# Optimization experiments

Measured on AMD Instinct MI355X. Metric: run time of the kernel, lower is better.

The kernel has to match this reference:

```python
import jax, jax.numpy as jnp
import numpy as np

B, T, I, H, F1, C = 65536, 30, 26, 24, 8, 4  # batch, seq_len, input, hidden, fc1, classes


def setup_inputs() -> dict:
    key = jax.random.key(0)
    ks = jax.random.split(key, 9)
    s_ih = 1.0 / np.sqrt(H)
    return {
        "x": jax.random.normal(ks[0], (B, T, I), dtype=jnp.float32),
        "W_ih": jax.random.uniform(ks[1], (3 * H, I), jnp.float32, -s_ih, s_ih),
        "W_hh": jax.random.uniform(ks[2], (3 * H, H), jnp.float32, -s_ih, s_ih),
        "b_ih": jax.random.uniform(ks[3], (3 * H,), jnp.float32, -s_ih, s_ih),
        "b_hh": jax.random.uniform(ks[4], (3 * H,), jnp.float32, -s_ih, s_ih),
        "fc1_w": jax.random.normal(ks[5], (F1, H), jnp.float32) * 0.1,
        "fc1_b": jax.random.normal(ks[6], (F1,), jnp.float32) * 0.1,
        "fc2_w": jax.random.normal(ks[7], (C, F1), jnp.float32) * 0.1,
        "fc2_b": jax.random.normal(ks[8], (C,), jnp.float32) * 0.1,
    }


def reference(x, W_ih, W_hh, b_ih, b_hh, fc1_w, fc1_b, fc2_w, fc2_b):
    # Precompute input projections for all timesteps: (B, T, 3H)
    xp = jnp.einsum("bti,gi->btg", x, W_ih) + b_ih

    def step(h, xt):  # h: (B,H), xt: (B,3H)
        gh = h @ W_hh.T + b_hh  # (B, 3H)
        xr, xz, xn = jnp.split(xt, 3, axis=-1)
        hr, hz, hn = jnp.split(gh, 3, axis=-1)
        r = jax.nn.sigmoid(xr + hr)
        z = jax.nn.sigmoid(xz + hz)
        n = jnp.tanh(xn + r * hn)
        h_new = (1.0 - z) * n + z * h
        return h_new, None

    h0 = jnp.zeros((x.shape[0], W_hh.shape[1]), dtype=x.dtype)
    h, _ = jax.lax.scan(step, h0, jnp.swapaxes(xp, 0, 1))  # final hidden (B, H)

    # eval mode: dropout is identity
    hid = jax.nn.relu(h @ fc1_w.T + fc1_b)
    logits = hid @ fc2_w.T + fc2_b
    return jax.nn.softmax(logits, axis=1)
```

## Files before the change

kernel.cpp:

```cpp
#include <hip/hip_runtime.h>

typedef __bf16 bf16x8 __attribute__((ext_vector_type(8)));
typedef float f32x4 __attribute__((ext_vector_type(4)));
typedef float f32x2 __attribute__((ext_vector_type(2)));

#define T_SEQ 30
#define NIN 26
#define XPITCH 780

#define W_IH 0
#define W_HH 1872
#define B_IH 3600
#define B_HH 3672
#define FC1W 3744
#define FC1B 3936
#define FC2W 3944
#define FC2B 3976

__device__ __forceinline__ float fast_sigmoid(float x) {
    return __builtin_amdgcn_rcpf(1.f + __expf(-x));
}
__device__ __forceinline__ float fast_tanh(float x) {
    return 2.f * __builtin_amdgcn_rcpf(1.f + __expf(-2.f * x)) - 1.f;
}

__global__ __launch_bounds__(256, 4) void gru_kernel(
    const float* __restrict__ x, const float* __restrict__ W_ih,
    const float* __restrict__ W_hh, const float* __restrict__ b_ih,
    const float* __restrict__ b_hh, const float* __restrict__ fc1_w,
    const float* __restrict__ fc1_b, const float* __restrict__ fc2_w,
    const float* __restrict__ fc2_b, float* __restrict__ out)
{
    __shared__ float wbuf[3980];
    __shared__ __attribute__((aligned(16))) __bf16 hbuf[4 * 512];

    const int tid = threadIdx.x;
    const int lane = tid & 63;
    const int wid = tid >> 6;
    const int m = lane & 15;
    const int kg = lane >> 4;
    const int w16 = wid << 4;
    const int b0 = blockIdx.x << 6;

    for (int i = tid; i < 1872; i += 256) wbuf[W_IH + i] = W_ih[i];
    for (int i = tid; i < 1728; i += 256) wbuf[W_HH + i] = W_hh[i];
    if (tid < 72) wbuf[B_IH + tid] = b_ih[tid];
    else if (tid < 144) wbuf[B_IH + tid] = b_hh[tid - 72];
    if (tid < 192) wbuf[FC1W + tid] = fc1_w[tid];
    if (tid < 8)   wbuf[FC1B + tid] = fc1_b[tid];
    if (tid < 32)  wbuf[FC2W + tid] = fc2_w[tid];
    if (tid < 4)   wbuf[FC2B + tid] = fc2_b[tid];
    for (int i = tid; i < 2048; i += 256) hbuf[i] = (__bf16)0.f;
    __syncthreads();

    bf16x8 bIh[6], bHh[6];
    float bxc[6], bhc[6];
    #pragma unroll
    for (int Tn = 0; Tn < 6; ++Tn) {
        const int np = Tn * 16 + m;
        const int gp = np >> 5;
        const int jh = np & 31;
        const bool vc = jh < 24;
        const int g = gp * 24 + jh;
        #pragma unroll
        for (int e = 0; e < 8; ++e) {
            const int k = kg * 8 + e;
            const float vi = (vc && k < 26) ? wbuf[W_IH + g * 26 + k] : 0.f;
            const float vh = (vc && k < 24) ? wbuf[W_HH + g * 24 + k] : 0.f;
            bIh[Tn][e] = (__bf16)vi;
            bHh[Tn][e] = (__bf16)vh;
        }
        bxc[Tn] = vc ? wbuf[B_IH + g] : 0.f;
        bhc[Tn] = vc ? wbuf[B_HH + g] : 0.f;
    }
    const float brz0 = bxc[0] + bhc[0], brz1 = bxc[1] + bhc[1];
    const float brz2 = bxc[2] + bhc[2], brz3 = bxc[3] + bhc[3];

    __bf16* hw = &hbuf[wid * 512];

    const float* px = x + (size_t)(b0 + w16 + m) * XPITCH + ((kg < 3) ? kg * 8 : 24);
    const bool full = (kg < 3);

    f32x2 zero2 = {0.f, 0.f};
    f32x2 xc0, xc1, xc2, xc3;
    xc1 = zero2; xc2 = zero2; xc3 = zero2;
    xc0 = *(const f32x2*)px;
    if (full) {
        xc1 = *(const f32x2*)(px + 2);
        xc2 = *(const f32x2*)(px + 4);
        xc3 = *(const f32x2*)(px + 6);
    }

    f32x4 hc0 = {0.f, 0.f, 0.f, 0.f}, hc1 = {0.f, 0.f, 0.f, 0.f};
    const f32x4 z4 = {0.f, 0.f, 0.f, 0.f};

    const int ra  = m * 32 + ((kg ^ (m >> 2)) << 3);
    const int wr0 = (kg * 4) * 32 + ((((m >> 3) ^ kg) & 3) << 3) + (m & 7);
    const int wr1 = (kg * 4) * 32 + (((2 ^ kg) & 3) << 3) + m;

    #pragma unroll 2
    for (int t = 0; t < T_SEQ; ++t) {
        f32x2 xn0, xn1, xn2, xn3;
        xn0 = zero2; xn1 = zero2; xn2 = zero2; xn3 = zero2;
        if (t < T_SEQ - 1) {
            const float* p = px + (t + 1) * NIN;
            xn0 = *(const f32x2*)p;
            if (full) {
                xn1 = *(const f32x2*)(p + 2);
                xn2 = *(const f32x2*)(p + 4);
                xn3 = *(const f32x2*)(p + 6);
            }
        }

        bf16x8 ax;
        ax[0] = (__bf16)xc0.x; ax[1] = (__bf16)xc0.y;
        ax[2] = (__bf16)xc1.x; ax[3] = (__bf16)xc1.y;
        ax[4] = (__bf16)xc2.x; ax[5] = (__bf16)xc2.y;
        ax[6] = (__bf16)xc3.x; ax[7] = (__bf16)xc3.y;

        const bf16x8 ah = *(const bf16x8*)&hw[ra];

        {
            f32x4 xr = __builtin_amdgcn_mfma_f32_16x16x32_bf16(ax, bIh[0], z4, 0, 0, 0);
            f32x4 hr = __builtin_amdgcn_mfma_f32_16x16x32_bf16(ah, bHh[0], z4, 0, 0, 0);
            f32x4 xz = __builtin_amdgcn_mfma_f32_16x16x32_bf16(ax, bIh[2], z4, 0, 0, 0);
            f32x4 hz = __builtin_amdgcn_mfma_f32_16x16x32_bf16(ah, bHh[2], z4, 0, 0, 0);
            f32x4 xn_ = __builtin_amdgcn_mfma_f32_16x16x32_bf16(ax, bIh[4], z4, 0, 0, 0);
            f32x4 hn = __builtin_amdgcn_mfma_f32_16x16x32_bf16(ah, bHh[4], z4, 0, 0, 0);
            #pragma unroll
            for (int r = 0; r < 4; ++r) {
                const float rg = fast_sigmoid(xr[r] + hr[r] + brz0);
                const float zg = fast_sigmoid(xz[r] + hz[r] + brz2);
                const float ng = fast_tanh(xn_[r] + bxc[4] + rg * (hn[r] + bhc[4]));
                hc0[r] = ng + zg * (hc0[r] - ng);
            }
            #pragma unroll
            for (int r = 0; r < 4; ++r)
                hw[wr0 + r * 32] = (__bf16)hc0[r];
        }

        {
            f32x4 xr = __builtin_amdgcn_mfma_f32_16x16x32_bf16(ax, bIh[1], z4, 0, 0, 0);
            f32x4 hr = __builtin_amdgcn_mfma_f32_16x16x32_bf16(ah, bHh[1], z4, 0, 0, 0);
            f32x4 xz = __builtin_amdgcn_mfma_f32_16x16x32_bf16(ax, bIh[3], z4, 0, 0, 0);
            f32x4 hz = __builtin_amdgcn_mfma_f32_16x16x32_bf16(ah, bHh[3], z4, 0, 0, 0);
            f32x4 xn_ = __builtin_amdgcn_mfma_f32_16x16x32_bf16(ax, bIh[5], z4, 0, 0, 0);
            f32x4 hn = __builtin_amdgcn_mfma_f32_16x16x32_bf16(ah, bHh[5], z4, 0, 0, 0);
            #pragma unroll
            for (int r = 0; r < 4; ++r) {
                const float rg = fast_sigmoid(xr[r] + hr[r] + brz1);
                const float zg = fast_sigmoid(xz[r] + hz[r] + brz3);
                const float ng = fast_tanh(xn_[r] + bxc[5] + rg * (hn[r] + bhc[5]));
                hc1[r] = ng + zg * (hc1[r] - ng);
            }
            if (m < 8) {
                #pragma unroll
                for (int r = 0; r < 4; ++r)
                    hw[wr1 + r * 32] = (__bf16)hc1[r];
            }
        }

        xc0 = xn0; xc1 = xn1; xc2 = xn2; xc3 = xn3;
    }

    if (lane < 16) {
        const int row = lane;
        float hv[24];
        #pragma unroll
        for (int j = 0; j < 24; ++j)
            hv[j] = (float)hw[row * 32 + ((((j >> 3) ^ (row >> 2)) & 3) << 3) + (j & 7)];
        float lg[4] = {wbuf[FC2B], wbuf[FC2B + 1], wbuf[FC2B + 2], wbuf[FC2B + 3]};
        #pragma unroll
        for (int o = 0; o < 8; ++o) {
            float s = wbuf[FC1B + o];
            #pragma unroll
            for (int j = 0; j < 24; ++j) s += wbuf[FC1W + o * 24 + j] * hv[j];
            s = fmaxf(s, 0.f);
            #pragma unroll
            for (int c = 0; c < 4; ++c) lg[c] += wbuf[FC2W + c * 8 + o] * s;
        }
        const float mx = fmaxf(fmaxf(lg[0], lg[1]), fmaxf(lg[2], lg[3]));
        const float e0 = __expf(lg[0] - mx), e1 = __expf(lg[1] - mx);
        const float e2 = __expf(lg[2] - mx), e3 = __expf(lg[3] - mx);
        const float inv = __builtin_amdgcn_rcpf(e0 + e1 + e2 + e3);
        f32x4 pr = {e0 * inv, e1 * inv, e2 * inv, e3 * inv};
        *(f32x4*)&out[(size_t)(b0 + w16 + row) * 4] = pr;
    }
}

extern "C" void kernel_launch(void* const* d_in, const int* in_sizes, int n_in,
                              void* d_out, int out_size, void* d_ws, size_t ws_size,
                              hipStream_t stream) {
    const float* xx    = (const float*)d_in[0];
    const float* w_ih  = (const float*)d_in[1];
    const float* w_hh  = (const float*)d_in[2];
    const float* bih   = (const float*)d_in[3];
    const float* bhh   = (const float*)d_in[4];
    const float* f1w   = (const float*)d_in[5];
    const float* f1b   = (const float*)d_in[6];
    const float* f2w   = (const float*)d_in[7];
    const float* f2b   = (const float*)d_in[8];
    float* outp = (float*)d_out;

    dim3 grid(65536 / 64), block(256);
    gru_kernel<<<grid, block, 0, stream>>>(xx, w_ih, w_hh, bih, bhh, f1w, f1b, f2w, f2b, outp);
}
```

Measured before the change: 323.0 us.

## Stage whole x tile into LDS as bf16 with coalesced loads, fold log2e

Instead of each lane fetching its x slice from global memory every timestep with strided 8-byte loads, the block cooperatively loads the entire 32-row x tile with contiguous row loads, converts it to bf16 and stores it in swizzled shared memory. The second half of the sequence is staged during the first timesteps to overlap loading with the recurrence. The block shrinks to 128 threads covering 32 rows, and weights are read directly from global memory instead of through LDS. Gate weights and biases are prescaled by log2e so sigmoid and tanh use a raw exp2 instruction. The cost is about 50KB of LDS per block, which limits occupancy, plus an extra barrier inside the time loop.

```diff
diff --git a/kernel.cpp b/kernel.cpp
--- a/kernel.cpp
+++ b/kernel.cpp
@@ -7,32 +7,46 @@
 #define T_SEQ 30
 #define NIN 26
 #define XPITCH 780
-
-#define W_IH 0
-#define W_HH 1872
-#define B_IH 3600
-#define B_HH 3672
-#define FC1W 3744
-#define FC1B 3936
-#define FC2W 3944
-#define FC2B 3976
-
-__device__ __forceinline__ float fast_sigmoid(float x) {
-    return __builtin_amdgcn_rcpf(1.f + __expf(-x));
+#define LOG2E 1.44269504088896340736f
+
+__device__ __forceinline__ float sig2(float s) {
+    return __builtin_amdgcn_rcpf(1.f + __builtin_amdgcn_exp2f(-s));
 }
-__device__ __forceinline__ float fast_tanh(float x) {
-    return 2.f * __builtin_amdgcn_rcpf(1.f + __expf(-2.f * x)) - 1.f;
-}
-
-__global__ __launch_bounds__(256, 4) void gru_kernel(
+
+#define LOADC(BUF, c, half) do {                                              \
+    const int rr_ = (c) / 15, tt_ = (c) % 15 + (half) * 15;                   \
+    const float* sp_ = x + (size_t)(b0 + rr_) * XPITCH + tt_ * NIN;           \
+    _Pragma("unroll") for (int q_ = 0; q_ < 13; ++q_)                         \
+        BUF[q_] = *(const f32x2*)(sp_ + 2 * q_);                              \
+} while (0)
+
+#define WRITEC(BUF, c, half) do {                                             \
+    const int rr_ = (c) / 15, tt_ = (c) % 15 + (half) * 15;                   \
+    const int id_ = rr_ * 30 + tt_;                                           \
+    const int ix_ = (id_ ^ ((rr_ >> 2) & 3)) << 3;                            \
+    _Pragma("unroll") for (int kk_ = 0; kk_ < 3; ++kk_) {                     \
+        bf16x8 wv_;                                                           \
+        _Pragma("unroll") for (int q_ = 0; q_ < 4; ++q_) {                    \
+            wv_[2 * q_]     = (__bf16)BUF[kk_ * 4 + q_].x;                    \
+            wv_[2 * q_ + 1] = (__bf16)BUF[kk_ * 4 + q_].y;                    \
+        }                                                                     \
+        *(bf16x8*)&xmain[kk_ * 7680 + ix_] = wv_;                             \
+    }                                                                         \
+    xtail[id_ * 2]     = (__bf16)BUF[12].x;                                   \
+    xtail[id_ * 2 + 1] = (__bf16)BUF[12].y;                                   \
+} while (0)
+
+__global__ __launch_bounds__(128, 2) void gru_kernel(
     const float* __restrict__ x, const float* __restrict__ W_ih,
     const float* __restrict__ W_hh, const float* __restrict__ b_ih,
     const float* __restrict__ b_hh, const float* __restrict__ fc1_w,
     const float* __restrict__ fc1_b, const float* __restrict__ fc2_w,
     const float* __restrict__ fc2_b, float* __restrict__ out)
 {
-    __shared__ float wbuf[3980];
-    __shared__ __attribute__((aligned(16))) __bf16 hbuf[4 * 512];
+    __shared__ __attribute__((aligned(16))) __bf16 xmain[23040];
+    __shared__ __attribute__((aligned(8)))  __bf16 xtail[1920];
+    __shared__ __attribute__((aligned(16))) __bf16 hbuf[1024];
+    __shared__ float wbuf[236];
 
     const int tid = threadIdx.x;
     const int lane = tid & 63;
@@ -40,23 +54,23 @@
     const int m = lane & 15;
     const int kg = lane >> 4;
     const int w16 = wid << 4;
-    const int b0 = blockIdx.x << 6;
-
-    for (int i = tid; i < 1872; i += 256) wbuf[W_IH + i] = W_ih[i];
-    for (int i = tid; i < 1728; i += 256) wbuf[W_HH + i] = W_hh[i];
-    if (tid < 72) wbuf[B_IH + tid] = b_ih[tid];
-    else if (tid < 144) wbuf[B_IH + tid] = b_hh[tid - 72];
-    if (tid < 192) wbuf[FC1W + tid] = fc1_w[tid];
-    if (tid < 8)   wbuf[FC1B + tid] = fc1_b[tid];
-    if (tid < 32)  wbuf[FC2W + tid] = fc2_w[tid];
-    if (tid < 4)   wbuf[FC2B + tid] = fc2_b[tid];
-    for (int i = tid; i < 2048; i += 256) hbuf[i] = (__bf16)0.f;
-    __syncthreads();
+    const int b0 = blockIdx.x << 5;
+
+    for (int i = tid; i < 236; i += 128) {
+        float v;
+        if (i < 192) v = fc1_w[i];
+        else if (i < 200) v = fc1_b[i - 192];
+        else if (i < 232) v = fc2_w[i - 200];
+        else v = fc2_b[i - 232];
+        wbuf[i] = v;
+    }
+    for (int i = tid; i < 1024; i += 128) hbuf[i] = (__bf16)0.f;
 
     bf16x8 bIh[6], bHh[6];
-    float bxc[6], bhc[6];
+    float bx[6], bh[6];
     #pragma unroll
     for (int Tn = 0; Tn < 6; ++Tn) {
+        const float sc = (Tn < 4) ? LOG2E : (2.f * LOG2E);
         const int np = Tn * 16 + m;
         const int gp = np >> 5;
         const int jh = np & 31;
@@ -65,59 +79,72 @@
         #pragma unroll
         for (int e = 0; e < 8; ++e) {
             const int k = kg * 8 + e;
-            const float vi = (vc && k < 26) ? wbuf[W_IH + g * 26 + k] : 0.f;
-            const float vh = (vc && k < 24) ? wbuf[W_HH + g * 24 + k] : 0.f;
-            bIh[Tn][e] = (__bf16)vi;
-            bHh[Tn][e] = (__bf16)vh;
-        }
-        bxc[Tn] = vc ? wbuf[B_IH + g] : 0.f;
-        bhc[Tn] = vc ? wbuf[B_HH + g] : 0.f;
-    }
-    const float brz0 = bxc[0] + bhc[0], brz1 = bxc[1] + bhc[1];
-    const float brz2 = bxc[2] + bhc[2], brz3 = bxc[3] + bhc[3];
-
-    __bf16* hw = &hbuf[wid * 512];
-
-    const float* px = x + (size_t)(b0 + w16 + m) * XPITCH + ((kg < 3) ? kg * 8 : 24);
-    const bool full = (kg < 3);
-
-    f32x2 zero2 = {0.f, 0.f};
-    f32x2 xc0, xc1, xc2, xc3;
-    xc1 = zero2; xc2 = zero2; xc3 = zero2;
-    xc0 = *(const f32x2*)px;
-    if (full) {
-        xc1 = *(const f32x2*)(px + 2);
-        xc2 = *(const f32x2*)(px + 4);
-        xc3 = *(const f32x2*)(px + 6);
-    }
-
-    f32x4 hc0 = {0.f, 0.f, 0.f, 0.f}, hc1 = {0.f, 0.f, 0.f, 0.f};
-    const f32x4 z4 = {0.f, 0.f, 0.f, 0.f};
-
+            bIh[Tn][e] = (__bf16)((vc && k < 26) ? W_ih[g * 26 + k] * sc : 0.f);
+            bHh[Tn][e] = (__bf16)((vc && k < 24) ? W_hh[g * 24 + k] * sc : 0.f);
+        }
+        bx[Tn] = vc ? b_ih[g] * sc : 0.f;
+        bh[Tn] = vc ? b_hh[g] * sc : 0.f;
+    }
+    const float brz0 = bx[0] + bh[0], brz1 = bx[1] + bh[1];
+    const float brz2 = bx[2] + bh[2], brz3 = bx[3] + bh[3];
+    const float bnx0 = bx[4], bnh0 = bh[4], bnx1 = bx[5], bnh1 = bh[5];
+
+    {
+        f32x2 bufA[13], bufB[13];
+        LOADC(bufA, tid, 0);
+        #pragma unroll
+        for (int j = 0; j < 4; ++j) {
+            if (j < 3) {
+                const int cn = tid + (j + 1) * 128;
+                if (cn < 480) LOADC(bufB, cn, 0);
+            }
+            const int cc = tid + j * 128;
+            if (cc < 480) WRITEC(bufA, cc, 0);
+            if (j < 3) {
+                #pragma unroll
+                for (int q = 0; q < 13; ++q) bufA[q] = bufB[q];
+            }
+        }
+    }
+    __syncthreads();
+
+    const int rowg = w16 + m;
+    const int sxr = (rowg >> 2) & 3;
+    const int rbase = rowg * 30;
     const int ra  = m * 32 + ((kg ^ (m >> 2)) << 3);
     const int wr0 = (kg * 4) * 32 + ((((m >> 3) ^ kg) & 3) << 3) + (m & 7);
     const int wr1 = (kg * 4) * 32 + (((2 ^ kg) & 3) << 3) + m;
-
-    #pragma unroll 2
+    __bf16* hw = &hbuf[wid * 512];
+
+    f32x4 hc0 = {0.f, 0.f, 0.f, 0.f}, hc1 = {0.f, 0.f, 0.f, 0.f};
+    const f32x4 z4 = {0.f, 0.f, 0.f, 0.f};
+    f32x2 bufS[13];
+
+    #pragma unroll 1
     for (int t = 0; t < T_SEQ; ++t) {
-        f32x2 xn0, xn1, xn2, xn3;
-        xn0 = zero2; xn1 = zero2; xn2 = zero2; xn3 = zero2;
-        if (t < T_SEQ - 1) {
-            const float* p = px + (t + 1) * NIN;
-            xn0 = *(const f32x2*)p;
-            if (full) {
-                xn1 = *(const f32x2*)(p + 2);
-                xn2 = *(const f32x2*)(p + 4);
-                xn3 = *(const f32x2*)(p + 6);
-            }
-        }
+        if (t >= 1 && t <= 8) {
+            if (t & 1) {
+                const int c = tid + (((t - 1) >> 1) << 7);
+                if (c < 480) LOADC(bufS, c, 1);
+            } else {
+                const int c = tid + (((t - 2) >> 1) << 7);
+                if (c < 480) WRITEC(bufS, c, 1);
+            }
+        }
+        if (t == 9) __syncthreads();
 
         bf16x8 ax;
-        ax[0] = (__bf16)xc0.x; ax[1] = (__bf16)xc0.y;
-        ax[2] = (__bf16)xc1.x; ax[3] = (__bf16)xc1.y;
-        ax[4] = (__bf16)xc2.x; ax[5] = (__bf16)xc2.y;
-        ax[6] = (__bf16)xc3.x; ax[7] = (__bf16)xc3.y;
-
+        {
+            const int id = rbase + t;
+            if (kg < 3) {
+                ax = *(const bf16x8*)&xmain[kg * 7680 + ((id ^ sxr) << 3)];
+            } else {
+                bf16x8 zz = {};
+                zz[0] = xtail[id * 2];
+                zz[1] = xtail[id * 2 + 1];
+                ax = zz;
+            }
+        }
         const bf16x8 ah = *(const bf16x8*)&hw[ra];
 
         {
@@ -125,13 +152,14 @@
             f32x4 hr = __builtin_amdgcn_mfma_f32_16x16x32_bf16(ah, bHh[0], z4, 0, 0, 0);
             f32x4 xz = __builtin_amdgcn_mfma_f32_16x16x32_bf16(ax, bIh[2], z4, 0, 0, 0);
             f32x4 hz = __builtin_amdgcn_mfma_f32_16x16x32_bf16(ah, bHh[2], z4, 0, 0, 0);
-            f32x4 xn_ = __builtin_amdgcn_mfma_f32_16x16x32_bf16(ax, bIh[4], z4, 0, 0, 0);
+            f32x4 xn = __builtin_amdgcn_mfma_f32_16x16x32_bf16(ax, bIh[4], z4, 0, 0, 0);
             f32x4 hn = __builtin_amdgcn_mfma_f32_16x16x32_bf16(ah, bHh[4], z4, 0, 0, 0);
             #pragma unroll
             for (int r = 0; r < 4; ++r) {
-                const float rg = fast_sigmoid(xr[r] + hr[r] + brz0);
-                const float zg = fast_sigmoid(xz[r] + hz[r] + brz2);
-                const float ng = fast_tanh(xn_[r] + bxc[4] + rg * (hn[r] + bhc[4]));
+                const float rg = sig2(xr[r] + hr[r] + brz0);
+                const float zg = sig2(xz[r] + hz[r] + brz2);
+                const float ag = xn[r] + bnx0 + rg * (hn[r] + bnh0);
+                const float ng = 2.f * sig2(ag) - 1.f;
                 hc0[r] = ng + zg * (hc0[r] - ng);
             }
             #pragma unroll
@@ -144,13 +172,14 @@
             f32x4 hr = __builtin_amdgcn_mfma_f32_16x16x32_bf16(ah, bHh[1], z4, 0, 0, 0);
             f32x4 xz = __builtin_amdgcn_mfma_f32_16x16x32_bf16(ax, bIh[3], z4, 0, 0, 0);
             f32x4 hz = __builtin_amdgcn_mfma_f32_16x16x32_bf16(ah, bHh[3], z4, 0, 0, 0);
-            f32x4 xn_ = __builtin_amdgcn_mfma_f32_16x16x32_bf16(ax, bIh[5], z4, 0, 0, 0);
+            f32x4 xn = __builtin_amdgcn_mfma_f32_16x16x32_bf16(ax, bIh[5], z4, 0, 0, 0);
             f32x4 hn = __builtin_amdgcn_mfma_f32_16x16x32_bf16(ah, bHh[5], z4, 0, 0, 0);
             #pragma unroll
             for (int r = 0; r < 4; ++r) {
-                const float rg = fast_sigmoid(xr[r] + hr[r] + brz1);
-                const float zg = fast_sigmoid(xz[r] + hz[r] + brz3);
-                const float ng = fast_tanh(xn_[r] + bxc[5] + rg * (hn[r] + bhc[5]));
+                const float rg = sig2(xr[r] + hr[r] + brz1);
+                const float zg = sig2(xz[r] + hz[r] + brz3);
+                const float ag = xn[r] + bnx1 + rg * (hn[r] + bnh1);
+                const float ng = 2.f * sig2(ag) - 1.f;
                 hc1[r] = ng + zg * (hc1[r] - ng);
             }
             if (m < 8) {
@@ -159,8 +188,6 @@
                     hw[wr1 + r * 32] = (__bf16)hc1[r];
             }
         }
-
-        xc0 = xn0; xc1 = xn1; xc2 = xn2; xc3 = xn3;
     }
 
     if (lane < 16) {
@@ -169,15 +196,15 @@
         #pragma unroll
         for (int j = 0; j < 24; ++j)
             hv[j] = (float)hw[row * 32 + ((((j >> 3) ^ (row >> 2)) & 3) << 3) + (j & 7)];
-        float lg[4] = {wbuf[FC2B], wbuf[FC2B + 1], wbuf[FC2B + 2], wbuf[FC2B + 3]};
+        float lg[4] = {wbuf[232], wbuf[233], wbuf[234], wbuf[235]};
         #pragma unroll
         for (int o = 0; o < 8; ++o) {
-            float s = wbuf[FC1B + o];
-            #pragma unroll
-            for (int j = 0; j < 24; ++j) s += wbuf[FC1W + o * 24 + j] * hv[j];
+            float s = wbuf[192 + o];
+            #pragma unroll
+            for (int j = 0; j < 24; ++j) s += wbuf[o * 24 + j] * hv[j];
             s = fmaxf(s, 0.f);
             #pragma unroll
-            for (int c = 0; c < 4; ++c) lg[c] += wbuf[FC2W + c * 8 + o] * s;
+            for (int c = 0; c < 4; ++c) lg[c] += wbuf[200 + c * 8 + o] * s;
         }
         const float mx = fmaxf(fmaxf(lg[0], lg[1]), fmaxf(lg[2], lg[3]));
         const float e0 = __expf(lg[0] - mx), e1 = __expf(lg[1] - mx);
@@ -202,6 +229,6 @@
     const float* f2b   = (const float*)d_in[8];
     float* outp = (float*)d_out;
 
-    dim3 grid(65536 / 64), block(256);
+    dim3 grid(65536 / 32), block(128);
     gru_kernel<<<grid, block, 0, stream>>>(xx, w_ih, w_hh, bih, bhh, f1w, f1b, f2w, f2b, outp);
 }
```

New measurement: 382.3 us. +18.4%, slower.
